# Kernel tuning notes

Measured on AMD Instinct MI355X. Metric: run time of the kernel, lower is better.

## Reference

```python
import jax, jax.numpy as jnp
import numpy as np

EPS = 1e-6
NUM_GROUPS = 32


def group_norm(x, w, b):
    # x: [B, C, W, H, L]
    B, C = x.shape[0], x.shape[1]
    xr = x.reshape(B, NUM_GROUPS, C // NUM_GROUPS, -1)
    mu = jnp.mean(xr, axis=(2, 3), keepdims=True)
    var = jnp.var(xr, axis=(2, 3), keepdims=True)
    xn = ((xr - mu) * jax.lax.rsqrt(var + EPS)).reshape(x.shape)
    return xn * w[None, :, None, None, None] + b[None, :, None, None, None]


def setup_inputs() -> dict:
    key = jax.random.key(0)
    ks = jax.random.split(key, 8)
    B, C, W, H, L = 2, 512, 16, 16, 16
    s = 1.0 / np.sqrt(C)
    return {
        "x": jax.random.normal(ks[0], (B, C, W, H, L), dtype=jnp.float32),
        "gn_w": jnp.ones((C,), dtype=jnp.float32),
        "gn_b": jnp.zeros((C,), dtype=jnp.float32),
        "q_w": jax.random.normal(ks[1], (C, C), dtype=jnp.float32) * s,
        "q_b": jnp.zeros((C,), dtype=jnp.float32),
        "k_w": jax.random.normal(ks[2], (C, C), dtype=jnp.float32) * s,
        "k_b": jnp.zeros((C,), dtype=jnp.float32),
        "v_w": jax.random.normal(ks[3], (C, C), dtype=jnp.float32) * s,
        "v_b": jnp.zeros((C,), dtype=jnp.float32),
        "p_w": jax.random.normal(ks[4], (C, C), dtype=jnp.float32) * s,
        "p_b": jnp.zeros((C,), dtype=jnp.float32),
    }


def reference(x, gn_w, gn_b, q_w, q_b, k_w, k_b, v_w, v_b, p_w, p_b):
    B, C, W, H, L = x.shape
    h = group_norm(x, gn_w, gn_b)
    hf = h.reshape(B, C, -1)  # [B, C, N]
    # 1x1 Conv3d == channel matmul: out[b,o,n] = sum_c w[o,c] * h[b,c,n] + b[o]
    q = jnp.einsum('oc,bcn->bon', q_w, hf) + q_b[None, :, None]
    k = jnp.einsum('oc,bcn->bon', k_w, hf) + k_b[None, :, None]
    v = jnp.einsum('oc,bcn->bon', v_w, hf) + v_b[None, :, None]
    scale = jnp.asarray(C, x.dtype) ** -0.5
    # w_[b,i,j] = sum_c q[b,c,i] * k[b,c,j]
    w_ = jnp.einsum('bci,bcj->bij', q, k) * scale
    w_ = jax.nn.softmax(w_, axis=2)
    # h_[b,c,i] = sum_j v[b,c,j] * w_[b,i,j]
    attn = jnp.einsum('bcj,bij->bci', v, w_)
    proj = jnp.einsum('oc,bcn->bon', p_w, attn) + p_b[None, :, None]
    return x + proj.reshape(B, C, W, H, L)
```

## Files before the change

### kernel.cpp

```cpp
#include <hip/hip_runtime.h>


typedef __bf16 bf16;
typedef __attribute__((ext_vector_type(8))) __bf16 bf16x8;
typedef __attribute__((ext_vector_type(4))) __bf16 bf16x4;
typedef __attribute__((ext_vector_type(4))) float f32x4;

#define CC 512
#define NN 4096
#define BM 128
#define BN 128
#define BK 64
#define SCALE_L2E 0.06376237870903338f

__device__ __forceinline__ void gload16(const bf16* g, bf16* l) {
    __builtin_amdgcn_global_load_lds(
        (const __attribute__((address_space(1))) unsigned int*)g,
        (__attribute__((address_space(3))) unsigned int*)l, 16, 0, 0);
}

__device__ __forceinline__ void gemm_core(
    const bf16* __restrict__ A, int lda,
    const bf16* __restrict__ B, int ldb,
    int kBeg, int kEnd, int m0, int n0, f32x4 acc[4][4])
{
    __shared__ __align__(16) bf16 Als[2][BM][BK];
    __shared__ __align__(16) bf16 Bls[2][BN][BK];
    const int t    = threadIdx.x;
    const int lane = t & 63;
    const int wid  = t >> 6;
    const int wm   = (wid >> 1) * 64;
    const int wn   = (wid & 1) * 64;
    const int fr   = lane & 15;
    const int kq   = lane >> 4;
    const int r_   = t >> 3;
    const int cbs  = (t & 7) ^ (r_ & 7);
    const int dcol = (t & 7) * 8;
    const int cs0  = ((kq)     ^ (fr & 7)) * 8;
    const int cs1  = ((kq + 4) ^ (fr & 7)) * 8;

    const bf16* Ab = A + (size_t)(m0 + r_) * lda + cbs * 8;
    const bf16* Bb = B + (size_t)(n0 + r_) * ldb + cbs * 8;

#define STAGE_G(bufi, kk) do {                                              \
        _Pragma("unroll")                                                   \
        for (int i = 0; i < 4; ++i)                                         \
            gload16(Ab + (kk) + (size_t)(i * 32) * lda,                     \
                    &Als[bufi][i * 32 + r_][dcol]);                         \
        _Pragma("unroll")                                                   \
        for (int i = 0; i < 4; ++i)                                         \
            gload16(Bb + (kk) + (size_t)(i * 32) * ldb,                     \
                    &Bls[bufi][i * 32 + r_][dcol]);                         \
    } while (0)

    int cur = 0;
    STAGE_G(0, kBeg);
    __syncthreads();
    for (int k0 = kBeg; k0 < kEnd; k0 += BK) {
        if (k0 + BK < kEnd) STAGE_G(cur ^ 1, k0 + BK);
        #pragma unroll
        for (int h = 0; h < 2; ++h) {
            const int cs = h ? cs1 : cs0;
            bf16x8 af[4], bg[4];
            #pragma unroll
            for (int f = 0; f < 4; ++f) {
                af[f] = *(const bf16x8*)&Als[cur][wm + f * 16 + fr][cs];
                bg[f] = *(const bf16x8*)&Bls[cur][wn + f * 16 + fr][cs];
            }
            #pragma unroll
            for (int fm = 0; fm < 4; ++fm)
                #pragma unroll
                for (int fn = 0; fn < 4; ++fn)
                    acc[fm][fn] = __builtin_amdgcn_mfma_f32_16x16x32_bf16(
                        af[fm], bg[fn], acc[fm][fn], 0, 0, 0);
        }
        __syncthreads();
        cur ^= 1;
    }
#undef STAGE_G
}

__device__ __forceinline__ void gemm_core64(
    const bf16* __restrict__ A, int lda,
    const bf16* __restrict__ B, int ldb,
    int kBeg, int kEnd, int m0, int n0, f32x4 acc[2][4])
{
    __shared__ __align__(16) bf16 Als[2][64][BK];
    __shared__ __align__(16) bf16 Bls[2][BN][BK];
    const int t    = threadIdx.x;
    const int lane = t & 63;
    const int wid  = t >> 6;
    const int wm   = (wid >> 1) * 32;
    const int wn   = (wid & 1) * 64;
    const int fr   = lane & 15;
    const int kq   = lane >> 4;
    const int r_   = t >> 3;
    const int cbs  = (t & 7) ^ (r_ & 7);
    const int dcol = (t & 7) * 8;
    const int cs0  = ((kq)     ^ (fr & 7)) * 8;
    const int cs1  = ((kq + 4) ^ (fr & 7)) * 8;

    const bf16* Ab = A + (size_t)(m0 + r_) * lda + cbs * 8;
    const bf16* Bb = B + (size_t)(n0 + r_) * ldb + cbs * 8;

#define STAGE_G64(bufi, kk) do {                                            \
        _Pragma("unroll")                                                   \
        for (int i = 0; i < 2; ++i)                                         \
            gload16(Ab + (kk) + (size_t)(i * 32) * lda,                     \
                    &Als[bufi][i * 32 + r_][dcol]);                         \
        _Pragma("unroll")                                                   \
        for (int i = 0; i < 4; ++i)                                         \
            gload16(Bb + (kk) + (size_t)(i * 32) * ldb,                     \
                    &Bls[bufi][i * 32 + r_][dcol]);                         \
    } while (0)

    int cur = 0;
    STAGE_G64(0, kBeg);
    __syncthreads();
    for (int k0 = kBeg; k0 < kEnd; k0 += BK) {
        if (k0 + BK < kEnd) STAGE_G64(cur ^ 1, k0 + BK);
        #pragma unroll
        for (int h = 0; h < 2; ++h) {
            const int cs = h ? cs1 : cs0;
            bf16x8 af[2], bg[4];
            #pragma unroll
            for (int f = 0; f < 2; ++f)
                af[f] = *(const bf16x8*)&Als[cur][wm + f * 16 + fr][cs];
            #pragma unroll
            for (int f = 0; f < 4; ++f)
                bg[f] = *(const bf16x8*)&Bls[cur][wn + f * 16 + fr][cs];
            #pragma unroll
            for (int fm = 0; fm < 2; ++fm)
                #pragma unroll
                for (int fn = 0; fn < 4; ++fn)
                    acc[fm][fn] = __builtin_amdgcn_mfma_f32_16x16x32_bf16(
                        af[fm], bg[fn], acc[fm][fn], 0, 0, 0);
        }
        __syncthreads();
        cur ^= 1;
    }
#undef STAGE_G64
}

__global__ __launch_bounds__(256) void convert_w_kernel(
    const float* __restrict__ qw, const float* __restrict__ kw,
    const float* __restrict__ pw, bf16* __restrict__ dst)
{
    const int which = blockIdx.y;
    const float* src = which == 0 ? qw : which == 1 ? kw : pw;
    const int slot  = which == 2 ? 3 : which;
    bf16* d = dst + (size_t)slot * (CC * CC);
    const int f4 = blockIdx.x * 256 + threadIdx.x;
    float4 v = ((const float4*)src)[f4];
    bf16x4 o;
    o[0] = (bf16)v.x; o[1] = (bf16)v.y; o[2] = (bf16)v.z; o[3] = (bf16)v.w;
    ((bf16x4*)d)[f4] = o;
}

__global__ __launch_bounds__(256) void vwT_kernel(
    const float* __restrict__ vw, bf16* __restrict__ vwT)
{
    const int k0 = blockIdx.x * 64;
    const int c0 = blockIdx.y * 64;
    const int t  = threadIdx.x;
    const int tk = t & 15, tc = t >> 4;
    float o[4][4];
    #pragma unroll
    for (int j = 0; j < 4; ++j) {
        const int c = c0 + tc * 4 + j;
        float4 v = *(const float4*)(vw + (size_t)c * CC + k0 + tk * 4);
        o[j][0] = v.x; o[j][1] = v.y; o[j][2] = v.z; o[j][3] = v.w;
    }
    #pragma unroll
    for (int i = 0; i < 4; ++i) {
        bf16x4 w4;
        w4[0] = (bf16)o[0][i]; w4[1] = (bf16)o[1][i];
        w4[2] = (bf16)o[2][i]; w4[3] = (bf16)o[3][i];
        *(bf16x4*)(vwT + (size_t)(k0 + tk * 4 + i) * CC + c0 + tc * 4) = w4;
    }
}

__global__ __launch_bounds__(256) void wb_kernel(
    const float* __restrict__ pw, const float* __restrict__ vb,
    float* __restrict__ wb)
{
    const int o = blockIdx.x * 256 + threadIdx.x;
    const float4* row = (const float4*)(pw + (size_t)o * CC);
    const float4* v4  = (const float4*)vb;
    float s = 0.f;
    #pragma unroll 4
    for (int i = 0; i < 128; ++i) {
        float4 a = row[i], b = v4[i];
        s += a.x * b.x + a.y * b.y + a.z * b.z + a.w * b.w;
    }
    wb[o] = s;
}

__global__ __launch_bounds__(256) void gn_stats_kernel(
    const float* __restrict__ x, float* __restrict__ mr)
{
    const int bg = blockIdx.x;
    const float4* base = (const float4*)(x + (size_t)bg * 16 * NN);
    const int t = threadIdx.x;
    float s = 0.f, sq = 0.f;
    #pragma unroll 4
    for (int i = 0; i < 64; ++i) {
        float4 v = base[i * 256 + t];
        s  += v.x + v.y + v.z + v.w;
        sq += v.x * v.x + v.y * v.y + v.z * v.z + v.w * v.w;
    }
    #pragma unroll
    for (int o = 32; o > 0; o >>= 1) { s += __shfl_xor(s, o); sq += __shfl_xor(sq, o); }
    __shared__ float rs[4], rq[4];
    const int lane = t & 63, wid = t >> 6;
    if (lane == 0) { rs[wid] = s; rq[wid] = sq; }
    __syncthreads();
    if (t == 0) {
        float S = rs[0] + rs[1] + rs[2] + rs[3];
        float Q = rq[0] + rq[1] + rq[2] + rq[3];
        const float invn = 1.f / 65536.f;
        float mean = S * invn;
        float var  = Q * invn - mean * mean;
        mr[bg * 2]     = mean;
        mr[bg * 2 + 1] = rsqrtf(var + 1e-6f);
    }
}

__global__ __launch_bounds__(256) void gn_apply_T_kernel(
    const float* __restrict__ x, const float* __restrict__ gw,
    const float* __restrict__ gb, const float* __restrict__ mr,
    bf16* __restrict__ hT)
{
    const int b  = blockIdx.z;
    const int n0 = blockIdx.x * 64;
    const int c0 = blockIdx.y * 64;
    const int t  = threadIdx.x;
    const int tn = t & 15, tc = t >> 4;
    float o[4][4];
    #pragma unroll
    for (int j = 0; j < 4; ++j) {
        const int c = c0 + tc * 4 + j;
        const int bg = b * 32 + (c >> 4);
        const float mean = mr[bg * 2], rstd = mr[bg * 2 + 1];
        const float w  = gw[c] * rstd;
        const float bb = gb[c] - mean * w;
        float4 v = *(const float4*)(x + ((size_t)(b * CC + c)) * NN + n0 + tn * 4);
        o[j][0] = v.x * w + bb; o[j][1] = v.y * w + bb;
        o[j][2] = v.z * w + bb; o[j][3] = v.w * w + bb;
    }
    bf16* dst = hT + (size_t)b * (size_t)NN * CC;
    #pragma unroll
    for (int i = 0; i < 4; ++i) {
        bf16x4 w4;
        w4[0] = (bf16)o[0][i]; w4[1] = (bf16)o[1][i];
        w4[2] = (bf16)o[2][i]; w4[3] = (bf16)o[3][i];
        *(bf16x4*)(dst + (size_t)(n0 + tn * 4 + i) * CC + c0 + tc * 4) = w4;
    }
}

__global__ __launch_bounds__(256) void qk_gemm_kernel(
    const bf16* __restrict__ hT, const bf16* __restrict__ wbf,
    const float* __restrict__ qb, const float* __restrict__ kb,
    bf16* __restrict__ qT, bf16* __restrict__ kT)
{
    const int z = blockIdx.z, b = z >> 1, w = z & 1;
    const size_t CN = (size_t)CC * NN;
    const bf16* A = hT + (size_t)b * CN;
    const bf16* B = wbf + (size_t)w * CC * CC;
    const float* bias = w ? kb : qb;
    bf16* outp = (w ? kT : qT) + (size_t)b * CN;
    const int m0 = blockIdx.y * BM, n0 = blockIdx.x * BN;
    f32x4 acc[4][4] = {};
    gemm_core(A, CC, B, CC, 0, CC, m0, n0, acc);
    const int lane = threadIdx.x & 63, wid = threadIdx.x >> 6;
    const int wm = (wid >> 1) * 64, wn = (wid & 1) * 64;
    const int cf = lane & 15, rb = (lane >> 4) * 4;
    #pragma unroll
    for (int fm = 0; fm < 4; ++fm)
      #pragma unroll
      for (int fn = 0; fn < 4; ++fn)
        #pragma unroll
        for (int r = 0; r < 4; ++r) {
            int row = m0 + wm + fm * 16 + rb + r;
            int col = n0 + wn + fn * 16 + cf;
            float val = acc[fm][fn][r] + bias[col];
            if (w == 0) val *= SCALE_L2E;
            outp[(size_t)row * CC + col] = (bf16)val;
        }
}

__global__ __launch_bounds__(256) void fw_gemm_kernel(
    const bf16* __restrict__ pwb, const bf16* __restrict__ vwT,
    bf16* __restrict__ fw)
{
    const int m0 = blockIdx.y * BM, n0 = blockIdx.x * BN;
    f32x4 acc[4][4] = {};
    gemm_core(pwb, CC, vwT, CC, 0, CC, m0, n0, acc);
    const int lane = threadIdx.x & 63, wid = threadIdx.x >> 6;
    const int wm = (wid >> 1) * 64, wn = (wid & 1) * 64;
    const int cf = lane & 15, rb = (lane >> 4) * 4;
    #pragma unroll
    for (int fm = 0; fm < 4; ++fm)
      #pragma unroll
      for (int fn = 0; fn < 4; ++fn)
        #pragma unroll
        for (int r = 0; r < 4; ++r)
            fw[(size_t)(m0 + wm + fm * 16 + rb + r) * CC
               + (n0 + wn + fn * 16 + cf)] = (bf16)acc[fm][fn][r];
}

__global__ __launch_bounds__(256) void w_gemm_kernel(
    const bf16* __restrict__ fw, const bf16* __restrict__ hT,
    bf16* __restrict__ Wt)
{
    const int b = blockIdx.z;
    const size_t CN = (size_t)CC * NN;
    const int m0 = blockIdx.y * 64, n0 = blockIdx.x * BN;
    f32x4 acc[2][4] = {};
    gemm_core64(fw, CC, hT + (size_t)b * CN, CC, 0, CC, m0, n0, acc);
    bf16* outp = Wt + (size_t)b * CN;
    const int lane = threadIdx.x & 63, wid = threadIdx.x >> 6;
    const int wm = (wid >> 1) * 32, wn = (wid & 1) * 64;
    const int cf = lane & 15, rb = (lane >> 4) * 4;
    #pragma unroll
    for (int fm = 0; fm < 2; ++fm)
      #pragma unroll
      for (int fn = 0; fn < 4; ++fn)
        #pragma unroll
        for (int r = 0; r < 4; ++r)
            outp[(size_t)(m0 + wm + fm * 16 + rb + r) * NN
                 + (n0 + wn + fn * 16 + cf)] = (bf16)acc[fm][fn][r];
}

__global__ __launch_bounds__(256) void se_gemm_kernel(
    const bf16* __restrict__ qT, const bf16* __restrict__ kT,
    bf16* __restrict__ E, float* __restrict__ rowsum)
{
    const int b = blockIdx.z;
    const size_t CN = (size_t)CC * NN;
    const bf16* qT_b = qT + (size_t)b * CN;
    const bf16* kT_b = kT + (size_t)b * CN;
    bf16* E_b = E + (size_t)b * NN * NN;
    float* rs_b = rowsum + (size_t)b * NN;
    const int m0 = blockIdx.y * BM, n0 = blockIdx.x * BN;
    f32x4 acc[4][4] = {};
    gemm_core(qT_b, CC, kT_b, CC, 0, CC, m0, n0, acc);
    const int lane = threadIdx.x & 63, wid = threadIdx.x >> 6;
    const int wm = (wid >> 1) * 64, wn = (wid & 1) * 64;
    const int cf = lane & 15, rb = (lane >> 4) * 4;
    #pragma unroll
    for (int fm = 0; fm < 4; ++fm)
      #pragma unroll
      for (int fn = 0; fn < 4; ++fn)
        #pragma unroll
        for (int r = 0; r < 4; ++r) {
            float e = exp2f(fminf(acc[fm][fn][r], 86.f));
            acc[fm][fn][r] = e;
            E_b[(size_t)(m0 + wm + fm * 16 + rb + r) * NN
                + (n0 + wn + fn * 16 + cf)] = (bf16)e;
        }
    #pragma unroll
    for (int fm = 0; fm < 4; ++fm)
      #pragma unroll
      for (int r = 0; r < 4; ++r) {
          float s = acc[fm][0][r] + acc[fm][1][r] + acc[fm][2][r] + acc[fm][3][r];
          s += __shfl_xor(s, 1); s += __shfl_xor(s, 2);
          s += __shfl_xor(s, 4); s += __shfl_xor(s, 8);
          if (cf == 0)
              atomicAdd(&rs_b[m0 + wm + fm * 16 + rb + r], s);
      }
}

__global__ __launch_bounds__(256) void pvproj_kernel(
    const bf16* __restrict__ Wt, const bf16* __restrict__ E,
    const float* __restrict__ rowsum, const float* __restrict__ wb,
    const float* __restrict__ pb, const float* __restrict__ x,
    float* __restrict__ outp)
{
    const int b = blockIdx.z;
    const size_t CN = (size_t)CC * NN;
    const int m0 = blockIdx.y * 64, n0 = blockIdx.x * BN;
    f32x4 acc[2][4] = {};
    gemm_core64(Wt + (size_t)b * CN, NN, E + (size_t)b * NN * NN, NN,
                0, NN, m0, n0, acc);
    const float* rs_b = rowsum + (size_t)b * NN;
    const int lane = threadIdx.x & 63, wid = threadIdx.x >> 6;
    const int wm = (wid >> 1) * 32, wn = (wid & 1) * 64;
    const int cf = lane & 15, rb = (lane >> 4) * 4;
    #pragma unroll
    for (int fm = 0; fm < 2; ++fm)
      #pragma unroll
      for (int fn = 0; fn < 4; ++fn) {
          const int col = n0 + wn + fn * 16 + cf;
          const float inv = 1.f / rs_b[col];
          #pragma unroll
          for (int r = 0; r < 4; ++r) {
              const int row = m0 + wm + fm * 16 + rb + r;
              const size_t idx = (size_t)b * CN + (size_t)row * NN + col;
              outp[idx] = acc[fm][fn][r] * inv + wb[row] + pb[row] + x[idx];
          }
      }
}

extern "C" void kernel_launch(void* const* d_in, const int* in_sizes, int n_in,
                              void* d_out, int out_size, void* d_ws, size_t ws_size,
                              hipStream_t stream)
{
    const float* x   = (const float*)d_in[0];
    const float* gnw = (const float*)d_in[1];
    const float* gnb = (const float*)d_in[2];
    const float* qw  = (const float*)d_in[3];
    const float* qb  = (const float*)d_in[4];
    const float* kw  = (const float*)d_in[5];
    const float* kb  = (const float*)d_in[6];
    const float* vw  = (const float*)d_in[7];
    const float* vb  = (const float*)d_in[8];
    const float* pw  = (const float*)d_in[9];
    const float* pb  = (const float*)d_in[10];
    float* outp = (float*)d_out;

    char* ws = (char*)d_ws;
    size_t off = 0;
    auto alloc = [&](size_t bytes) -> char* {
        char* p = ws + off;
        off = (off + bytes + 255) & ~(size_t)255;
        return p;
    };
    const size_t CN = (size_t)CC * NN;
    bf16*  wbf  = (bf16*)alloc(4 * (size_t)CC * CC * sizeof(bf16));
    bf16*  hT   = (bf16*)alloc(2 * CN * sizeof(bf16));
    bf16*  qT   = (bf16*)alloc(2 * CN * sizeof(bf16));
    bf16*  kT   = (bf16*)alloc(2 * CN * sizeof(bf16));
    bf16*  fw   = (bf16*)alloc((size_t)CC * CC * sizeof(bf16));
    bf16*  Wt   = (bf16*)alloc(2 * CN * sizeof(bf16));
    bf16*  E    = (bf16*)alloc(2 * (size_t)NN * NN * sizeof(bf16));
    float* rowsum = (float*)alloc(2 * NN * sizeof(float));
    float* wb   = (float*)alloc(CC * sizeof(float));
    float* mr   = (float*)alloc(64 * 2 * sizeof(float));

    bf16* vwT = wbf + 2 * (size_t)CC * CC;
    bf16* pwb = wbf + 3 * (size_t)CC * CC;

    convert_w_kernel<<<dim3(256, 3), 256, 0, stream>>>(qw, kw, pw, wbf);
    vwT_kernel<<<dim3(8, 8), 256, 0, stream>>>(vw, vwT);
    wb_kernel<<<2, 256, 0, stream>>>(pw, vb, wb);
    gn_stats_kernel<<<64, 256, 0, stream>>>(x, mr);
    gn_apply_T_kernel<<<dim3(NN / 64, CC / 64, 2), 256, 0, stream>>>(
        x, gnw, gnb, mr, hT);
    hipMemsetAsync(rowsum, 0, 2 * NN * sizeof(float), stream);

    fw_gemm_kernel<<<dim3(4, 4), 256, 0, stream>>>(pwb, vwT, fw);
    qk_gemm_kernel<<<dim3(CC / BN, NN / BM, 4), 256, 0, stream>>>(
        hT, wbf, qb, kb, qT, kT);
    w_gemm_kernel<<<dim3(NN / BN, 8, 2), 256, 0, stream>>>(fw, hT, Wt);

    se_gemm_kernel<<<dim3(NN / BN, NN / BM, 2), 256, 0, stream>>>(
        qT, kT, E, rowsum);

    pvproj_kernel<<<dim3(NN / BN, 8, 2), 256, 0, stream>>>(
        Wt, E, rowsum, wb, pb, x, outp);
}
```

Measured before the change: 206.7 us.

## Add triple-buffered 512-thread GEMM core and retile attention GEMMs onto it

Adds a new GEMM core with a three-stage LDS ring buffer, explicit vmcnt waits and raw s_barrier, so global-to-LDS loads run two stages ahead of the MFMA work. The qk, w, se and pvproj kernels move to 512-thread blocks with larger tiles (256x128 or 128x128), a 2x4 wave layout, and launch_bounds(512,2). The goal is to hide memory latency and improve reuse per block in the dominant GEMMs, at the cost of more LDS per block, higher register pressure, and fewer blocks in the grid.

Result: slower. 222.6 us (+7.7%).

```diff
diff --git a/kernel.cpp b/kernel.cpp
--- a/kernel.cpp
+++ b/kernel.cpp
@@ -17,6 +17,74 @@
     __builtin_amdgcn_global_load_lds(
         (const __attribute__((address_space(1))) unsigned int*)g,
         (__attribute__((address_space(3))) unsigned int*)l, 16, 0, 0);
+}
+
+template<int FA, int NSTEP>
+__device__ __forceinline__ void core_p3(
+    const bf16* __restrict__ A, int lda,
+    const bf16* __restrict__ B, int ldb,
+    int m0, int n0, f32x4 acc[FA][2])
+{
+    constexpr int BMt  = FA * 32;
+    constexpr int ROWS = BMt + 128;
+    constexpr int L    = ROWS / 64;
+    __shared__ __align__(16) bf16 ls[3][ROWS][BK];
+
+    const int t    = threadIdx.x;
+    const int lane = t & 63;
+    const int wid  = t >> 6;
+    const int wm   = (wid >> 2) * (FA * 16);
+    const int wn   = (wid & 3) * 32;
+    const int fr   = lane & 15;
+    const int kq   = lane >> 4;
+    const int cs0  = ((kq)     ^ (fr & 7)) * 8;
+    const int cs1  = ((kq + 4) ^ (fr & 7)) * 8;
+
+    auto STAGE = [&](int bi, int kk) {
+        #pragma unroll
+        for (int j = 0; j < L; ++j) {
+            const int idx = t + j * 512;
+            const int row = idx >> 3;
+            const int blk = (idx & 7) ^ (row & 7);
+            const bf16* g = (row < BMt)
+                ? A + (size_t)(m0 + row) * lda + kk + blk * 8
+                : B + (size_t)(n0 + row - BMt) * ldb + kk + blk * 8;
+            gload16(g, &ls[bi][row][(idx & 7) * 8]);
+        }
+    };
+
+    STAGE(0, 0);
+    STAGE(1, BK);
+    for (int i = 0; i < NSTEP; ++i) {
+        if (i + 2 < NSTEP) {
+            STAGE((i + 2) % 3, (i + 2) * BK);
+            asm volatile("s_waitcnt vmcnt(%0)" :: "n"(2 * L) : "memory");
+        } else if (i + 1 < NSTEP) {
+            asm volatile("s_waitcnt vmcnt(%0)" :: "n"(L) : "memory");
+        } else {
+            asm volatile("s_waitcnt vmcnt(0)" ::: "memory");
+        }
+        __builtin_amdgcn_s_barrier();
+        const int bi = i % 3;
+        #pragma unroll
+        for (int h = 0; h < 2; ++h) {
+            const int cs = h ? cs1 : cs0;
+            bf16x8 af[FA], bg[2];
+            #pragma unroll
+            for (int f = 0; f < FA; ++f)
+                af[f] = *(const bf16x8*)&ls[bi][wm + f * 16 + fr][cs];
+            #pragma unroll
+            for (int g = 0; g < 2; ++g)
+                bg[g] = *(const bf16x8*)&ls[bi][BMt + wn + g * 16 + fr][cs];
+            #pragma unroll
+            for (int fm = 0; fm < FA; ++fm)
+                #pragma unroll
+                for (int g = 0; g < 2; ++g)
+                    acc[fm][g] = __builtin_amdgcn_mfma_f32_16x16x32_bf16(
+                        af[fm], bg[g], acc[fm][g], 0, 0, 0);
+        }
+        __builtin_amdgcn_s_barrier();
+    }
 }
 
 __device__ __forceinline__ void gemm_core(
@@ -80,68 +148,6 @@
 #undef STAGE_G
 }
 
-__device__ __forceinline__ void gemm_core64(
-    const bf16* __restrict__ A, int lda,
-    const bf16* __restrict__ B, int ldb,
-    int kBeg, int kEnd, int m0, int n0, f32x4 acc[2][4])
-{
-    __shared__ __align__(16) bf16 Als[2][64][BK];
-    __shared__ __align__(16) bf16 Bls[2][BN][BK];
-    const int t    = threadIdx.x;
-    const int lane = t & 63;
-    const int wid  = t >> 6;
-    const int wm   = (wid >> 1) * 32;
-    const int wn   = (wid & 1) * 64;
-    const int fr   = lane & 15;
-    const int kq   = lane >> 4;
-    const int r_   = t >> 3;
-    const int cbs  = (t & 7) ^ (r_ & 7);
-    const int dcol = (t & 7) * 8;
-    const int cs0  = ((kq)     ^ (fr & 7)) * 8;
-    const int cs1  = ((kq + 4) ^ (fr & 7)) * 8;
-
-    const bf16* Ab = A + (size_t)(m0 + r_) * lda + cbs * 8;
-    const bf16* Bb = B + (size_t)(n0 + r_) * ldb + cbs * 8;
-
-#define STAGE_G64(bufi, kk) do {                                            \
-        _Pragma("unroll")                                                   \
-        for (int i = 0; i < 2; ++i)                                         \
-            gload16(Ab + (kk) + (size_t)(i * 32) * lda,                     \
-                    &Als[bufi][i * 32 + r_][dcol]);                         \
-        _Pragma("unroll")                                                   \
-        for (int i = 0; i < 4; ++i)                                         \
-            gload16(Bb + (kk) + (size_t)(i * 32) * ldb,                     \
-                    &Bls[bufi][i * 32 + r_][dcol]);                         \
-    } while (0)
-
-    int cur = 0;
-    STAGE_G64(0, kBeg);
-    __syncthreads();
-    for (int k0 = kBeg; k0 < kEnd; k0 += BK) {
-        if (k0 + BK < kEnd) STAGE_G64(cur ^ 1, k0 + BK);
-        #pragma unroll
-        for (int h = 0; h < 2; ++h) {
-            const int cs = h ? cs1 : cs0;
-            bf16x8 af[2], bg[4];
-            #pragma unroll
-            for (int f = 0; f < 2; ++f)
-                af[f] = *(const bf16x8*)&Als[cur][wm + f * 16 + fr][cs];
-            #pragma unroll
-            for (int f = 0; f < 4; ++f)
-                bg[f] = *(const bf16x8*)&Bls[cur][wn + f * 16 + fr][cs];
-            #pragma unroll
-            for (int fm = 0; fm < 2; ++fm)
-                #pragma unroll
-                for (int fn = 0; fn < 4; ++fn)
-                    acc[fm][fn] = __builtin_amdgcn_mfma_f32_16x16x32_bf16(
-                        af[fm], bg[fn], acc[fm][fn], 0, 0, 0);
-        }
-        __syncthreads();
-        cur ^= 1;
-    }
-#undef STAGE_G64
-}
-
 __global__ __launch_bounds__(256) void convert_w_kernel(
     const float* __restrict__ qw, const float* __restrict__ kw,
     const float* __restrict__ pw, bf16* __restrict__ dst)
@@ -258,7 +264,27 @@
     }
 }
 
-__global__ __launch_bounds__(256) void qk_gemm_kernel(
+__global__ __launch_bounds__(256) void fw_gemm_kernel(
+    const bf16* __restrict__ pwb, const bf16* __restrict__ vwT,
+    bf16* __restrict__ fw)
+{
+    const int m0 = blockIdx.y * BM, n0 = blockIdx.x * BN;
+    f32x4 acc[4][4] = {};
+    gemm_core(pwb, CC, vwT, CC, 0, CC, m0, n0, acc);
+    const int lane = threadIdx.x & 63, wid = threadIdx.x >> 6;
+    const int wm = (wid >> 1) * 64, wn = (wid & 1) * 64;
+    const int cf = lane & 15, rb = (lane >> 4) * 4;
+    #pragma unroll
+    for (int fm = 0; fm < 4; ++fm)
+      #pragma unroll
+      for (int fn = 0; fn < 4; ++fn)
+        #pragma unroll
+        for (int r = 0; r < 4; ++r)
+            fw[(size_t)(m0 + wm + fm * 16 + rb + r) * CC
+               + (n0 + wn + fn * 16 + cf)] = (bf16)acc[fm][fn][r];
+}
+
+__global__ __launch_bounds__(512, 2) void qk_gemm_kernel(
     const bf16* __restrict__ hT, const bf16* __restrict__ wbf,
     const float* __restrict__ qb, const float* __restrict__ kb,
     bf16* __restrict__ qT, bf16* __restrict__ kT)
@@ -269,70 +295,50 @@
     const bf16* B = wbf + (size_t)w * CC * CC;
     const float* bias = w ? kb : qb;
     bf16* outp = (w ? kT : qT) + (size_t)b * CN;
-    const int m0 = blockIdx.y * BM, n0 = blockIdx.x * BN;
-    f32x4 acc[4][4] = {};
-    gemm_core(A, CC, B, CC, 0, CC, m0, n0, acc);
+    const int m0 = blockIdx.y * 256, n0 = blockIdx.x * 128;
+    f32x4 acc[8][2] = {};
+    core_p3<8, CC / BK>(A, CC, B, CC, m0, n0, acc);
     const int lane = threadIdx.x & 63, wid = threadIdx.x >> 6;
-    const int wm = (wid >> 1) * 64, wn = (wid & 1) * 64;
+    const int wm = (wid >> 2) * 128, wn = (wid & 3) * 32;
     const int cf = lane & 15, rb = (lane >> 4) * 4;
     #pragma unroll
-    for (int fm = 0; fm < 4; ++fm)
-      #pragma unroll
-      for (int fn = 0; fn < 4; ++fn)
+    for (int fm = 0; fm < 8; ++fm)
+      #pragma unroll
+      for (int g = 0; g < 2; ++g)
         #pragma unroll
         for (int r = 0; r < 4; ++r) {
             int row = m0 + wm + fm * 16 + rb + r;
-            int col = n0 + wn + fn * 16 + cf;
-            float val = acc[fm][fn][r] + bias[col];
+            int col = n0 + wn + g * 16 + cf;
+            float val = acc[fm][g][r] + bias[col];
             if (w == 0) val *= SCALE_L2E;
             outp[(size_t)row * CC + col] = (bf16)val;
         }
 }
 
-__global__ __launch_bounds__(256) void fw_gemm_kernel(
-    const bf16* __restrict__ pwb, const bf16* __restrict__ vwT,
-    bf16* __restrict__ fw)
-{
-    const int m0 = blockIdx.y * BM, n0 = blockIdx.x * BN;
-    f32x4 acc[4][4] = {};
-    gemm_core(pwb, CC, vwT, CC, 0, CC, m0, n0, acc);
-    const int lane = threadIdx.x & 63, wid = threadIdx.x >> 6;
-    const int wm = (wid >> 1) * 64, wn = (wid & 1) * 64;
-    const int cf = lane & 15, rb = (lane >> 4) * 4;
-    #pragma unroll
-    for (int fm = 0; fm < 4; ++fm)
-      #pragma unroll
-      for (int fn = 0; fn < 4; ++fn)
-        #pragma unroll
-        for (int r = 0; r < 4; ++r)
-            fw[(size_t)(m0 + wm + fm * 16 + rb + r) * CC
-               + (n0 + wn + fn * 16 + cf)] = (bf16)acc[fm][fn][r];
-}
-
-__global__ __launch_bounds__(256) void w_gemm_kernel(
+__global__ __launch_bounds__(512, 2) void w_gemm_kernel(
     const bf16* __restrict__ fw, const bf16* __restrict__ hT,
     bf16* __restrict__ Wt)
 {
     const int b = blockIdx.z;
     const size_t CN = (size_t)CC * NN;
-    const int m0 = blockIdx.y * 64, n0 = blockIdx.x * BN;
-    f32x4 acc[2][4] = {};
-    gemm_core64(fw, CC, hT + (size_t)b * CN, CC, 0, CC, m0, n0, acc);
+    const int m0 = blockIdx.y * 128, n0 = blockIdx.x * 128;
+    f32x4 acc[4][2] = {};
+    core_p3<4, CC / BK>(fw, CC, hT + (size_t)b * CN, CC, m0, n0, acc);
     bf16* outp = Wt + (size_t)b * CN;
     const int lane = threadIdx.x & 63, wid = threadIdx.x >> 6;
-    const int wm = (wid >> 1) * 32, wn = (wid & 1) * 64;
+    const int wm = (wid >> 2) * 64, wn = (wid & 3) * 32;
     const int cf = lane & 15, rb = (lane >> 4) * 4;
     #pragma unroll
-    for (int fm = 0; fm < 2; ++fm)
-      #pragma unroll
-      for (int fn = 0; fn < 4; ++fn)
+    for (int fm = 0; fm < 4; ++fm)
+      #pragma unroll
+      for (int g = 0; g < 2; ++g)
         #pragma unroll
         for (int r = 0; r < 4; ++r)
             outp[(size_t)(m0 + wm + fm * 16 + rb + r) * NN
-                 + (n0 + wn + fn * 16 + cf)] = (bf16)acc[fm][fn][r];
-}
-
-__global__ __launch_bounds__(256) void se_gemm_kernel(
+                 + (n0 + wn + g * 16 + cf)] = (bf16)acc[fm][g][r];
+}
+
+__global__ __launch_bounds__(512, 2) void se_gemm_kernel(
     const bf16* __restrict__ qT, const bf16* __restrict__ kT,
     bf16* __restrict__ E, float* __restrict__ rowsum)
 {
@@ -342,28 +348,28 @@
     const bf16* kT_b = kT + (size_t)b * CN;
     bf16* E_b = E + (size_t)b * NN * NN;
     float* rs_b = rowsum + (size_t)b * NN;
-    const int m0 = blockIdx.y * BM, n0 = blockIdx.x * BN;
-    f32x4 acc[4][4] = {};
-    gemm_core(qT_b, CC, kT_b, CC, 0, CC, m0, n0, acc);
+    const int m0 = blockIdx.y * 256, n0 = blockIdx.x * 128;
+    f32x4 acc[8][2] = {};
+    core_p3<8, CC / BK>(qT_b, CC, kT_b, CC, m0, n0, acc);
     const int lane = threadIdx.x & 63, wid = threadIdx.x >> 6;
-    const int wm = (wid >> 1) * 64, wn = (wid & 1) * 64;
+    const int wm = (wid >> 2) * 128, wn = (wid & 3) * 32;
     const int cf = lane & 15, rb = (lane >> 4) * 4;
     #pragma unroll
-    for (int fm = 0; fm < 4; ++fm)
-      #pragma unroll
-      for (int fn = 0; fn < 4; ++fn)
+    for (int fm = 0; fm < 8; ++fm)
+      #pragma unroll
+      for (int g = 0; g < 2; ++g)
         #pragma unroll
         for (int r = 0; r < 4; ++r) {
-            float e = exp2f(fminf(acc[fm][fn][r], 86.f));
-            acc[fm][fn][r] = e;
+            float e = exp2f(fminf(acc[fm][g][r], 86.f));
+            acc[fm][g][r] = e;
             E_b[(size_t)(m0 + wm + fm * 16 + rb + r) * NN
-                + (n0 + wn + fn * 16 + cf)] = (bf16)e;
-        }
-    #pragma unroll
-    for (int fm = 0; fm < 4; ++fm)
+                + (n0 + wn + g * 16 + cf)] = (bf16)e;
+        }
+    #pragma unroll
+    for (int fm = 0; fm < 8; ++fm)
       #pragma unroll
       for (int r = 0; r < 4; ++r) {
-          float s = acc[fm][0][r] + acc[fm][1][r] + acc[fm][2][r] + acc[fm][3][r];
+          float s = acc[fm][0][r] + acc[fm][1][r];
           s += __shfl_xor(s, 1); s += __shfl_xor(s, 2);
           s += __shfl_xor(s, 4); s += __shfl_xor(s, 8);
           if (cf == 0)
@@ -371,7 +377,7 @@
       }
 }
 
-__global__ __launch_bounds__(256) void pvproj_kernel(
+__global__ __launch_bounds__(512, 2) void pvproj_kernel(
     const bf16* __restrict__ Wt, const bf16* __restrict__ E,
     const float* __restrict__ rowsum, const float* __restrict__ wb,
     const float* __restrict__ pb, const float* __restrict__ x,
@@ -379,25 +385,25 @@
 {
     const int b = blockIdx.z;
     const size_t CN = (size_t)CC * NN;
-    const int m0 = blockIdx.y * 64, n0 = blockIdx.x * BN;
-    f32x4 acc[2][4] = {};
-    gemm_core64(Wt + (size_t)b * CN, NN, E + (size_t)b * NN * NN, NN,
-                0, NN, m0, n0, acc);
+    const int m0 = blockIdx.y * 128, n0 = blockIdx.x * 128;
+    f32x4 acc[4][2] = {};
+    core_p3<4, NN / BK>(Wt + (size_t)b * CN, NN,
+                        E + (size_t)b * NN * NN, NN, m0, n0, acc);
     const float* rs_b = rowsum + (size_t)b * NN;
     const int lane = threadIdx.x & 63, wid = threadIdx.x >> 6;
-    const int wm = (wid >> 1) * 32, wn = (wid & 1) * 64;
+    const int wm = (wid >> 2) * 64, wn = (wid & 3) * 32;
     const int cf = lane & 15, rb = (lane >> 4) * 4;
     #pragma unroll
-    for (int fm = 0; fm < 2; ++fm)
-      #pragma unroll
-      for (int fn = 0; fn < 4; ++fn) {
-          const int col = n0 + wn + fn * 16 + cf;
+    for (int fm = 0; fm < 4; ++fm)
+      #pragma unroll
+      for (int g = 0; g < 2; ++g) {
+          const int col = n0 + wn + g * 16 + cf;
           const float inv = 1.f / rs_b[col];
           #pragma unroll
           for (int r = 0; r < 4; ++r) {
               const int row = m0 + wm + fm * 16 + rb + r;
               const size_t idx = (size_t)b * CN + (size_t)row * NN + col;
-              outp[idx] = acc[fm][fn][r] * inv + wb[row] + pb[row] + x[idx];
+              outp[idx] = acc[fm][g][r] * inv + wb[row] + pb[row] + x[idx];
           }
       }
 }
@@ -450,13 +456,13 @@
     hipMemsetAsync(rowsum, 0, 2 * NN * sizeof(float), stream);
 
     fw_gemm_kernel<<<dim3(4, 4), 256, 0, stream>>>(pwb, vwT, fw);
-    qk_gemm_kernel<<<dim3(CC / BN, NN / BM, 4), 256, 0, stream>>>(
+    qk_gemm_kernel<<<dim3(CC / 128, NN / 256, 4), 512, 0, stream>>>(
         hT, wbf, qb, kb, qT, kT);
-    w_gemm_kernel<<<dim3(NN / BN, 8, 2), 256, 0, stream>>>(fw, hT, Wt);
-
-    se_gemm_kernel<<<dim3(NN / BN, NN / BM, 2), 256, 0, stream>>>(
+    w_gemm_kernel<<<dim3(NN / 128, CC / 128, 2), 512, 0, stream>>>(fw, hT, Wt);
+
+    se_gemm_kernel<<<dim3(NN / 128, NN / 256, 2), 512, 0, stream>>>(
         qT, kT, E, rowsum);
 
-    pvproj_kernel<<<dim3(NN / BN, 8, 2), 256, 0, stream>>>(
+    pvproj_kernel<<<dim3(NN / 128, CC / 128, 2), 512, 0, stream>>>(
         Wt, E, rowsum, wb, pb, x, outp);
 }
```

## Merge QK and W GEMMs into one launch, split GN stats, remap blocks for XCDs

Applied to the files above, without the earlier changes.

The group-norm statistics pass now splits each group across four blocks and accumulates sums with atomics. The apply kernel derives mean and rstd from those sums. The separate Q/K and W projection GEMMs become a single 768-block launch using 128x128 tiles, which removes one kernel launch and fills the GPU better. The attention-score and PV/proj kernels now use a 1D grid with an (id&7)*k + id>>3 remap, so neighbouring tiles land on the same XCD and share L2. The cost is an extra memset and atomic accumulation in the stats pass, plus a branchy role dispatch in the fused GEMM.

Measured after the change: 213.0 us. 1.03x slower.

```diff
diff --git a/kernel.cpp b/kernel.cpp
--- a/kernel.cpp
+++ b/kernel.cpp
@@ -199,13 +199,14 @@
 __global__ __launch_bounds__(256) void gn_stats_kernel(
     const float* __restrict__ x, float* __restrict__ mr)
 {
-    const int bg = blockIdx.x;
+    const int bg = blockIdx.x >> 2;
+    const int qq = blockIdx.x & 3;
     const float4* base = (const float4*)(x + (size_t)bg * 16 * NN);
     const int t = threadIdx.x;
     float s = 0.f, sq = 0.f;
     #pragma unroll 4
-    for (int i = 0; i < 64; ++i) {
-        float4 v = base[i * 256 + t];
+    for (int i = 0; i < 16; ++i) {
+        float4 v = base[(qq * 16 + i) * 256 + t];
         s  += v.x + v.y + v.z + v.w;
         sq += v.x * v.x + v.y * v.y + v.z * v.z + v.w * v.w;
     }
@@ -216,13 +217,8 @@
     if (lane == 0) { rs[wid] = s; rq[wid] = sq; }
     __syncthreads();
     if (t == 0) {
-        float S = rs[0] + rs[1] + rs[2] + rs[3];
-        float Q = rq[0] + rq[1] + rq[2] + rq[3];
-        const float invn = 1.f / 65536.f;
-        float mean = S * invn;
-        float var  = Q * invn - mean * mean;
-        mr[bg * 2]     = mean;
-        mr[bg * 2 + 1] = rsqrtf(var + 1e-6f);
+        atomicAdd(&mr[bg * 2],     rs[0] + rs[1] + rs[2] + rs[3]);
+        atomicAdd(&mr[bg * 2 + 1], rq[0] + rq[1] + rq[2] + rq[3]);
     }
 }
 
@@ -241,7 +237,10 @@
     for (int j = 0; j < 4; ++j) {
         const int c = c0 + tc * 4 + j;
         const int bg = b * 32 + (c >> 4);
-        const float mean = mr[bg * 2], rstd = mr[bg * 2 + 1];
+        const float invn = 1.f / 65536.f;
+        const float mean = mr[bg * 2] * invn;
+        const float var  = mr[bg * 2 + 1] * invn - mean * mean;
+        const float rstd = rsqrtf(var + 1e-6f);
         const float w  = gw[c] * rstd;
         const float bb = gb[c] - mean * w;
         float4 v = *(const float4*)(x + ((size_t)(b * CC + c)) * NN + n0 + tn * 4);
@@ -256,37 +255,6 @@
         w4[2] = (bf16)o[2][i]; w4[3] = (bf16)o[3][i];
         *(bf16x4*)(dst + (size_t)(n0 + tn * 4 + i) * CC + c0 + tc * 4) = w4;
     }
-}
-
-__global__ __launch_bounds__(256) void qk_gemm_kernel(
-    const bf16* __restrict__ hT, const bf16* __restrict__ wbf,
-    const float* __restrict__ qb, const float* __restrict__ kb,
-    bf16* __restrict__ qT, bf16* __restrict__ kT)
-{
-    const int z = blockIdx.z, b = z >> 1, w = z & 1;
-    const size_t CN = (size_t)CC * NN;
-    const bf16* A = hT + (size_t)b * CN;
-    const bf16* B = wbf + (size_t)w * CC * CC;
-    const float* bias = w ? kb : qb;
-    bf16* outp = (w ? kT : qT) + (size_t)b * CN;
-    const int m0 = blockIdx.y * BM, n0 = blockIdx.x * BN;
-    f32x4 acc[4][4] = {};
-    gemm_core(A, CC, B, CC, 0, CC, m0, n0, acc);
-    const int lane = threadIdx.x & 63, wid = threadIdx.x >> 6;
-    const int wm = (wid >> 1) * 64, wn = (wid & 1) * 64;
-    const int cf = lane & 15, rb = (lane >> 4) * 4;
-    #pragma unroll
-    for (int fm = 0; fm < 4; ++fm)
-      #pragma unroll
-      for (int fn = 0; fn < 4; ++fn)
-        #pragma unroll
-        for (int r = 0; r < 4; ++r) {
-            int row = m0 + wm + fm * 16 + rb + r;
-            int col = n0 + wn + fn * 16 + cf;
-            float val = acc[fm][fn][r] + bias[col];
-            if (w == 0) val *= SCALE_L2E;
-            outp[(size_t)row * CC + col] = (bf16)val;
-        }
 }
 
 __global__ __launch_bounds__(256) void fw_gemm_kernel(
@@ -309,40 +277,72 @@
                + (n0 + wn + fn * 16 + cf)] = (bf16)acc[fm][fn][r];
 }
 
-__global__ __launch_bounds__(256) void w_gemm_kernel(
-    const bf16* __restrict__ fw, const bf16* __restrict__ hT,
-    bf16* __restrict__ Wt)
-{
-    const int b = blockIdx.z;
+__global__ __launch_bounds__(256) void qkw_gemm_kernel(
+    const bf16* __restrict__ hT, const bf16* __restrict__ wbf,
+    const bf16* __restrict__ fw,
+    const float* __restrict__ qb, const float* __restrict__ kb,
+    bf16* __restrict__ qT, bf16* __restrict__ kT, bf16* __restrict__ Wt)
+{
     const size_t CN = (size_t)CC * NN;
-    const int m0 = blockIdx.y * 64, n0 = blockIdx.x * BN;
-    f32x4 acc[2][4] = {};
-    gemm_core64(fw, CC, hT + (size_t)b * CN, CC, 0, CC, m0, n0, acc);
-    bf16* outp = Wt + (size_t)b * CN;
+    int id = blockIdx.x;
+    id = (id & 7) * 96 + (id >> 3);
+    const int seg = id >> 7, s = id & 127;
+
+    const bf16* A; const bf16* B;
+    int m0, n0, ldo; bf16* outp; const float* bias; int role;
+    if (seg < 4) {
+        role = seg & 1;
+        const int b = seg >> 1;
+        A = hT + (size_t)b * CN;
+        B = wbf + (size_t)role * CC * CC;
+        m0 = (s >> 2) * 128; n0 = (s & 3) * 128;
+        outp = (role ? kT : qT) + (size_t)b * CN; ldo = CC;
+        bias = role ? kb : qb;
+    } else {
+        role = 2;
+        const int b = seg - 4;
+        A = fw;
+        B = hT + (size_t)b * CN;
+        m0 = (s >> 5) * 128; n0 = (s & 31) * 128;
+        outp = Wt + (size_t)b * CN; ldo = NN;
+        bias = nullptr;
+    }
+    f32x4 acc[4][4] = {};
+    gemm_core(A, CC, B, CC, 0, CC, m0, n0, acc);
     const int lane = threadIdx.x & 63, wid = threadIdx.x >> 6;
-    const int wm = (wid >> 1) * 32, wn = (wid & 1) * 64;
+    const int wm = (wid >> 1) * 64, wn = (wid & 1) * 64;
     const int cf = lane & 15, rb = (lane >> 4) * 4;
     #pragma unroll
-    for (int fm = 0; fm < 2; ++fm)
+    for (int fm = 0; fm < 4; ++fm)
       #pragma unroll
-      for (int fn = 0; fn < 4; ++fn)
-        #pragma unroll
-        for (int r = 0; r < 4; ++r)
-            outp[(size_t)(m0 + wm + fm * 16 + rb + r) * NN
-                 + (n0 + wn + fn * 16 + cf)] = (bf16)acc[fm][fn][r];
+      for (int fn = 0; fn < 4; ++fn) {
+          const int col = n0 + wn + fn * 16 + cf;
+          const float bv = (role < 2) ? bias[col] : 0.f;
+          #pragma unroll
+          for (int r = 0; r < 4; ++r) {
+              const int row = m0 + wm + fm * 16 + rb + r;
+              float val = acc[fm][fn][r] + bv;
+              if (role == 0) val *= SCALE_L2E;
+              outp[(size_t)row * ldo + col] = (bf16)val;
+          }
+      }
 }
 
 __global__ __launch_bounds__(256) void se_gemm_kernel(
     const bf16* __restrict__ qT, const bf16* __restrict__ kT,
     bf16* __restrict__ E, float* __restrict__ rowsum)
 {
-    const int b = blockIdx.z;
+    int id = blockIdx.x;
+    int b = 0;
+    if (id >= 1024) { b = 1; id -= 1024; }
+    id = (id & 7) * 128 + (id >> 3);
+    const int m0 = (id >> 5) * 128, n0 = (id & 31) * 128;
+
     const size_t CN = (size_t)CC * NN;
     const bf16* qT_b = qT + (size_t)b * CN;
     const bf16* kT_b = kT + (size_t)b * CN;
     bf16* E_b = E + (size_t)b * NN * NN;
     float* rs_b = rowsum + (size_t)b * NN;
-    const int m0 = blockIdx.y * BM, n0 = blockIdx.x * BN;
     f32x4 acc[4][4] = {};
     gemm_core(qT_b, CC, kT_b, CC, 0, CC, m0, n0, acc);
     const int lane = threadIdx.x & 63, wid = threadIdx.x >> 6;
@@ -377,12 +377,17 @@
     const float* __restrict__ pb, const float* __restrict__ x,
     float* __restrict__ outp)
 {
-    const int b = blockIdx.z;
+    int id = blockIdx.x;
+    int b = 0;
+    if (id >= 256) { b = 1; id -= 256; }
+    id = (id & 7) * 32 + (id >> 3);
+    const int m0 = (id & 7) * 64;
+    const int n0 = (id >> 3) * 128;
+
     const size_t CN = (size_t)CC * NN;
-    const int m0 = blockIdx.y * 64, n0 = blockIdx.x * BN;
     f32x4 acc[2][4] = {};
-    gemm_core64(Wt + (size_t)b * CN, NN, E + (size_t)b * NN * NN, NN,
-                0, NN, m0, n0, acc);
+    gemm_core64(Wt + (size_t)b * CN, NN,
+                E + (size_t)b * NN * NN, NN, 0, NN, m0, n0, acc);
     const float* rs_b = rowsum + (size_t)b * NN;
     const int lane = threadIdx.x & 63, wid = threadIdx.x >> 6;
     const int wm = (wid >> 1) * 32, wn = (wid & 1) * 64;
@@ -390,14 +395,14 @@
     #pragma unroll
     for (int fm = 0; fm < 2; ++fm)
       #pragma unroll
-      for (int fn = 0; fn < 4; ++fn) {
-          const int col = n0 + wn + fn * 16 + cf;
+      for (int g = 0; g < 4; ++g) {
+          const int col = n0 + wn + g * 16 + cf;
           const float inv = 1.f / rs_b[col];
           #pragma unroll
           for (int r = 0; r < 4; ++r) {
               const int row = m0 + wm + fm * 16 + rb + r;
               const size_t idx = (size_t)b * CN + (size_t)row * NN + col;
-              outp[idx] = acc[fm][fn][r] * inv + wb[row] + pb[row] + x[idx];
+              outp[idx] = acc[fm][g][r] * inv + wb[row] + pb[row] + x[idx];
           }
       }
 }
@@ -444,19 +449,18 @@
     convert_w_kernel<<<dim3(256, 3), 256, 0, stream>>>(qw, kw, pw, wbf);
     vwT_kernel<<<dim3(8, 8), 256, 0, stream>>>(vw, vwT);
     wb_kernel<<<2, 256, 0, stream>>>(pw, vb, wb);
-    gn_stats_kernel<<<64, 256, 0, stream>>>(x, mr);
+    hipMemsetAsync(mr, 0, 64 * 2 * sizeof(float), stream);
+    gn_stats_kernel<<<256, 256, 0, stream>>>(x, mr);
     gn_apply_T_kernel<<<dim3(NN / 64, CC / 64, 2), 256, 0, stream>>>(
         x, gnw, gnb, mr, hT);
     hipMemsetAsync(rowsum, 0, 2 * NN * sizeof(float), stream);
 
     fw_gemm_kernel<<<dim3(4, 4), 256, 0, stream>>>(pwb, vwT, fw);
-    qk_gemm_kernel<<<dim3(CC / BN, NN / BM, 4), 256, 0, stream>>>(
-        hT, wbf, qb, kb, qT, kT);
-    w_gemm_kernel<<<dim3(NN / BN, 8, 2), 256, 0, stream>>>(fw, hT, Wt);
-
-    se_gemm_kernel<<<dim3(NN / BN, NN / BM, 2), 256, 0, stream>>>(
-        qT, kT, E, rowsum);
-
-    pvproj_kernel<<<dim3(NN / BN, 8, 2), 256, 0, stream>>>(
+    qkw_gemm_kernel<<<768, 256, 0, stream>>>(
+        hT, wbf, fw, qb, kb, qT, kT, Wt);
+
+    se_gemm_kernel<<<2048, 256, 0, stream>>>(qT, kT, E, rowsum);
+
+    pvproj_kernel<<<512, 256, 0, stream>>>(
         Wt, E, rowsum, wb, pb, x, outp);
 }
```
